# Kernel tuning notes

Measured on AMD Instinct MI355X. Metric: run time of the kernel, lower is better.

The kernel has to match this reference:

```python
import jax, jax.numpy as jnp
import numpy as np

B, S, D = 4, 4096, 1024
STATE = 1024
HID = 4 * D
EPS_NORM = 1e-6           # RMSNorm module eps
EPS_FP32 = 1.1920929e-7   # torch F.rms_norm default eps = finfo(fp32).eps


def rms_norm(x, eps):
    # no learned weight (RMSNorm(dim=-1) has weight=None)
    return x * jax.lax.rsqrt(jnp.mean(jnp.square(x), axis=-1, keepdims=True) + eps)


def setup_inputs() -> dict:
    key = jax.random.key(0)
    ks = jax.random.split(key, 8)
    scale_d = 1.0 / np.sqrt(D)
    scale_s = 1.0 / np.sqrt(STATE)
    scale_h = 1.0 / np.sqrt(HID)
    return {
        "x": jax.random.normal(ks[0], (B, S, D), jnp.float32),
        "x0": jax.random.normal(ks[1], (B, S, D), jnp.float32),
        "Wu": jax.random.normal(ks[2], (STATE, D), jnp.float32) * scale_d,
        "Wg": jax.random.normal(ks[3], (STATE, D), jnp.float32) * scale_d,
        "Wo": jax.random.normal(ks[4], (D, STATE), jnp.float32) * scale_s,
        "Wfc": jax.random.normal(ks[5], (HID, D), jnp.float32) * scale_d,
        "Wproj": jax.random.normal(ks[6], (D, HID), jnp.float32) * scale_h,
        "memory_mix": jnp.ones((D,), jnp.float32),
        "mlp_scale": jnp.ones((D,), jnp.float32),
        "resid_mix": jnp.stack([jnp.ones((D,), jnp.float32), jnp.zeros((D,), jnp.float32)]),
    }


def reference(x, x0, Wu, Wg, Wo, Wfc, Wproj, memory_mix, mlp_scale, resid_mix):
    # residual mix of x and x0
    x = resid_mix[0][None, None, :] * x + resid_mix[1][None, None, :] * x0

    # --- CausalPrefixMemory branch ---
    h = rms_norm(x, EPS_NORM)
    update = jnp.einsum('bsd,kd->bsk', h, Wu)
    gate = jax.nn.sigmoid(jnp.einsum('bsd,kd->bsk', h, Wg))
    memory = jnp.cumsum(gate * update, axis=1)          # [B,S,STATE]
    denom = jnp.arange(1, S + 1, dtype=jnp.float32)[None, :, None]
    m = rms_norm(memory / denom, EPS_FP32)
    mem_out = jnp.einsum('bsk,dk->bsd', m, Wo)
    x = x + memory_mix[None, None, :] * mem_out

    # --- MLP branch: relu^2 ---
    h2 = rms_norm(x, EPS_NORM)
    r = jax.nn.relu(jnp.einsum('bsd,hd->bsh', h2, Wfc))
    mlp_out = jnp.einsum('bsh,dh->bsd', jnp.square(r), Wproj)
    x = x + mlp_scale[None, None, :] * mlp_out
    return x
```

## Files before the change

kernel.cpp:

```cpp
#include <hip/hip_runtime.h>
#include <stdint.h>

typedef unsigned short u16;
typedef __attribute__((ext_vector_type(8))) short s16x8;
typedef __attribute__((ext_vector_type(4))) float f32x4;

__device__ __forceinline__ u16 f2bf(float f) {
  uint32_t u = __float_as_uint(f);
  uint32_t r = (u + 0x7FFFu + ((u >> 16) & 1u)) >> 16;
  return (u16)r;
}

__device__ __forceinline__ void gll16(const void* g, void* lds) {
  __builtin_amdgcn_global_load_lds(
      (const __attribute__((address_space(1))) uint32_t*)g,
      (__attribute__((address_space(3))) uint32_t*)lds, 16, 0, 0);
}

__device__ __forceinline__ void xcd_swz(int& bx, int& by) {
  int gx = gridDim.x;
  int lin = blockIdx.y * gx + blockIdx.x;
  int cpx = (gx * gridDim.y) >> 3;
  int nl = (lin & 7) * cpx + (lin >> 3);
  bx = nl % gx;
  by = nl / gx;
}

__global__ __launch_bounds__(256) void k_f2b(const float* __restrict__ src,
                                             u16* __restrict__ dst, int n) {
  int i = (blockIdx.x * 256 + threadIdx.x) * 4;
  if (i < n) {
    float4 v = *(const float4*)(src + i);
    ushort4 o;
    o.x = f2bf(v.x); o.y = f2bf(v.y); o.z = f2bf(v.z); o.w = f2bf(v.w);
    *(ushort4*)(dst + i) = o;
  }
}

template <bool MIX>
__global__ __launch_bounds__(256) void k_rms(const float* __restrict__ X,
                                             const float* __restrict__ X0,
                                             const float* __restrict__ rmix,
                                             float* __restrict__ XMout,
                                             u16* __restrict__ Hout, float eps) {
  const int row = blockIdx.x, t = threadIdx.x;
  const size_t base = (size_t)row * 1024;
  float4 v;
  if (MIX) {
    float4 a = ((const float4*)(X + base))[t];
    float4 b = ((const float4*)(X0 + base))[t];
    float4 c0 = ((const float4*)rmix)[t];
    float4 c1 = ((const float4*)(rmix + 1024))[t];
    v.x = c0.x * a.x + c1.x * b.x;
    v.y = c0.y * a.y + c1.y * b.y;
    v.z = c0.z * a.z + c1.z * b.z;
    v.w = c0.w * a.w + c1.w * b.w;
  } else {
    v = ((const float4*)(X + base))[t];
  }
  float ss = v.x * v.x + v.y * v.y + v.z * v.z + v.w * v.w;
#pragma unroll
  for (int o = 32; o > 0; o >>= 1) ss += __shfl_xor(ss, o);
  __shared__ float red[4];
  if ((t & 63) == 0) red[t >> 6] = ss;
  __syncthreads();
  float tot = red[0] + red[1] + red[2] + red[3];
  float sc = rsqrtf(tot * (1.0f / 1024.0f) + eps);
  if (MIX) ((float4*)(XMout + base))[t] = v;
  ushort4 hv;
  hv.x = f2bf(v.x * sc); hv.y = f2bf(v.y * sc);
  hv.z = f2bf(v.z * sc); hv.w = f2bf(v.w * sc);
  ((ushort4*)(Hout + base))[t] = hv;
}

__global__ __launch_bounds__(256) void k_scan2(float* __restrict__ CS) {
  int idx = blockIdx.x * 256 + threadIdx.x;
  int b = idx >> 10, k = idx & 1023;
  float run = 0.f;
  for (int c = 0; c < 256; ++c) {
    size_t o = ((size_t)b * 256 + c) * 1024 + k;
    float v = CS[o];
    CS[o] = run;
    run += v;
  }
}

__global__ __launch_bounds__(64) void k_scan3f(const float* __restrict__ P,
                                               const float* __restrict__ CS,
                                               u16* __restrict__ Mout) {
  int blk = blockIdx.x;
  int chunk = blk & 255, b = blk >> 8;
  const int t = threadIdx.x;
  const float4* cs4 = (const float4*)(CS + ((size_t)b * 256 + chunk) * 1024);
  float4 run[4];
#pragma unroll
  for (int q = 0; q < 4; ++q) run[q] = cs4[q * 64 + t];
  const float4* p4 = (const float4*)(P + ((size_t)b * 4096 + chunk * 16) * 1024);
  u16* mo = Mout + ((size_t)b * 4096 + chunk * 16) * 1024;
  const int rowbase = chunk * 16;
#pragma unroll 2
  for (int i = 0; i < 16; ++i) {
    float4 v[4];
#pragma unroll
    for (int q = 0; q < 4; ++q) v[q] = p4[(size_t)i * 256 + q * 64 + t];
    const float inv = 1.0f / (float)(rowbase + i + 1);
    float4 y[4];
    float ss = 0.f;
#pragma unroll
    for (int q = 0; q < 4; ++q) {
      run[q].x += v[q].x; run[q].y += v[q].y;
      run[q].z += v[q].z; run[q].w += v[q].w;
      y[q].x = run[q].x * inv; y[q].y = run[q].y * inv;
      y[q].z = run[q].z * inv; y[q].w = run[q].w * inv;
      ss += y[q].x * y[q].x + y[q].y * y[q].y
          + y[q].z * y[q].z + y[q].w * y[q].w;
    }
#pragma unroll
    for (int o = 32; o > 0; o >>= 1) ss += __shfl_xor(ss, o);
    float sc = rsqrtf(ss * (1.0f / 1024.0f) + 1.1920929e-7f);
#pragma unroll
    for (int q = 0; q < 4; ++q) {
      ushort4 hv;
      hv.x = f2bf(y[q].x * sc); hv.y = f2bf(y[q].y * sc);
      hv.z = f2bf(y[q].z * sc); hv.w = f2bf(y[q].w * sc);
      *(ushort4*)(mo + (size_t)i * 1024 + (q * 64 + t) * 4) = hv;
    }
  }
}

__global__ __launch_bounds__(256, 2) void gemm_dual(
    const u16* __restrict__ A, const u16* __restrict__ Bu,
    const u16* __restrict__ Bg, float* __restrict__ P,
    float* __restrict__ CS, int K) {
  __shared__ __align__(16) u16 As[128 * 64];
  __shared__ __align__(16) u16 Us[64 * 64];
  __shared__ __align__(16) u16 Gs[64 * 64];
  const int t = threadIdx.x;
  const int lane = t & 63, wid = t >> 6;
  int bx, by;
  xcd_swz(bx, by);
  const int m0 = by * 128, n0 = bx * 64;
  const int wm = wid * 32;
  const int l15 = lane & 15, lhi = lane >> 4;

  size_t gA[4], gU[2];
#pragma unroll
  for (int i = 0; i < 4; ++i) {
    int j = i * 256 + t;
    int row = j >> 3;
    int k16 = (j & 7) ^ (row & 7);
    gA[i] = (size_t)(m0 + row) * K + k16 * 8;
  }
#pragma unroll
  for (int i = 0; i < 2; ++i) {
    int j = i * 256 + t;
    int row = j >> 3;
    int k16 = (j & 7) ^ (row & 7);
    gU[i] = (size_t)(n0 + row) * K + k16 * 8;
  }

  f32x4 au[2][4], ag[2][4];
#pragma unroll
  for (int mi = 0; mi < 2; ++mi)
#pragma unroll
    for (int ni = 0; ni < 4; ++ni) { au[mi][ni] = 0.0f; ag[mi][ni] = 0.0f; }

  for (int kb = 0; kb < K; kb += 64) {
#pragma unroll
    for (int i = 0; i < 4; ++i) {
      int j = i * 256 + t;
      gll16(A + gA[i] + kb, &As[j * 8]);
    }
#pragma unroll
    for (int i = 0; i < 2; ++i) {
      int j = i * 256 + t;
      gll16(Bu + gU[i] + kb, &Us[j * 8]);
      gll16(Bg + gU[i] + kb, &Gs[j * 8]);
    }
    __syncthreads();
#pragma unroll
    for (int kc = 0; kc < 2; ++kc) {
      s16x8 af[2], uf[4], gf[4];
#pragma unroll
      for (int mi = 0; mi < 2; ++mi) {
        int row = wm + mi * 16 + l15;
        int k16 = (kc * 4 + lhi) ^ (row & 7);
        af[mi] = *(const s16x8*)&As[row * 64 + k16 * 8];
      }
#pragma unroll
      for (int ni = 0; ni < 4; ++ni) {
        int row = ni * 16 + l15;
        int k16 = (kc * 4 + lhi) ^ (row & 7);
        uf[ni] = *(const s16x8*)&Us[row * 64 + k16 * 8];
        gf[ni] = *(const s16x8*)&Gs[row * 64 + k16 * 8];
      }
#pragma unroll
      for (int mi = 0; mi < 2; ++mi)
#pragma unroll
        for (int ni = 0; ni < 4; ++ni) {
          au[mi][ni] = __builtin_amdgcn_mfma_f32_16x16x32_bf16(
              af[mi], uf[ni], au[mi][ni], 0, 0, 0);
          ag[mi][ni] = __builtin_amdgcn_mfma_f32_16x16x32_bf16(
              af[mi], gf[ni], ag[mi][ni], 0, 0, 0);
        }
    }
    __syncthreads();
  }

#pragma unroll
  for (int mi = 0; mi < 2; ++mi) {
    int r0 = m0 + wm + mi * 16 + lhi * 4;
#pragma unroll
    for (int ni = 0; ni < 4; ++ni) {
      int c = n0 + ni * 16 + l15;
      float ps = 0.f;
#pragma unroll
      for (int j = 0; j < 4; ++j) {
        float u = au[mi][ni][j], g = ag[mi][ni][j];
        float p = u / (1.0f + __expf(-g));
        P[(size_t)(r0 + j) * 1024 + c] = p;
        ps += p;
      }
      ps += __shfl_xor(ps, 16);
      ps += __shfl_xor(ps, 32);
      if (lhi == 0) {
        int grow = m0 + wm + mi * 16;
        int b = grow >> 12;
        int chunk = (grow & 4095) >> 4;
        CS[((size_t)b * 256 + chunk) * 1024 + c] = ps;
      }
    }
  }
}

template <int EPI>
__global__ __launch_bounds__(256, 2) void gemm_bf16(
    const u16* __restrict__ A, const u16* __restrict__ Bw, void* __restrict__ Cout,
    const float* __restrict__ Cadd, const float* __restrict__ colscale,
    int K, int lda, int ldb, int ldc) {
  __shared__ __align__(16) u16 As[128 * 64];
  __shared__ __align__(16) u16 Bs[128 * 64];
  const int t = threadIdx.x;
  const int lane = t & 63, wid = t >> 6;
  int bx, by;
  xcd_swz(bx, by);
  const int m0 = by * 128, n0 = bx * 128;
  const int wm = (wid >> 1) * 64, wn = (wid & 1) * 64;
  const int l15 = lane & 15, lhi = lane >> 4;

  size_t gA[4], gB[4];
#pragma unroll
  for (int i = 0; i < 4; ++i) {
    int j = i * 256 + t;
    int row = j >> 3;
    int k16 = (j & 7) ^ (row & 7);
    gA[i] = (size_t)(m0 + row) * lda + k16 * 8;
    gB[i] = (size_t)(n0 + row) * ldb + k16 * 8;
  }

  f32x4 acc[4][4];
#pragma unroll
  for (int mi = 0; mi < 4; ++mi)
#pragma unroll
    for (int ni = 0; ni < 4; ++ni) acc[mi][ni] = 0.0f;

  for (int kb = 0; kb < K; kb += 64) {
#pragma unroll
    for (int i = 0; i < 4; ++i) {
      int j = i * 256 + t;
      gll16(A + gA[i] + kb, &As[j * 8]);
      gll16(Bw + gB[i] + kb, &Bs[j * 8]);
    }
    __syncthreads();
#pragma unroll
    for (int kc = 0; kc < 2; ++kc) {
      s16x8 af[4], bfr[4];
#pragma unroll
      for (int mi = 0; mi < 4; ++mi) {
        int row = wm + mi * 16 + l15;
        int k16 = (kc * 4 + lhi) ^ (row & 7);
        af[mi] = *(const s16x8*)&As[row * 64 + k16 * 8];
      }
#pragma unroll
      for (int ni = 0; ni < 4; ++ni) {
        int row = wn + ni * 16 + l15;
        int k16 = (kc * 4 + lhi) ^ (row & 7);
        bfr[ni] = *(const s16x8*)&Bs[row * 64 + k16 * 8];
      }
#pragma unroll
      for (int mi = 0; mi < 4; ++mi)
#pragma unroll
        for (int ni = 0; ni < 4; ++ni)
          acc[mi][ni] = __builtin_amdgcn_mfma_f32_16x16x32_bf16(
              af[mi], bfr[ni], acc[mi][ni], 0, 0, 0);
    }
    __syncthreads();
  }

#pragma unroll
  for (int mi = 0; mi < 4; ++mi) {
    int r0 = m0 + wm + mi * 16 + lhi * 4;
#pragma unroll
    for (int ni = 0; ni < 4; ++ni) {
      int c = n0 + wn + ni * 16 + l15;
      float cs = (EPI == 1) ? colscale[c] : 0.f;
#pragma unroll
      for (int j = 0; j < 4; ++j) {
        size_t idx = (size_t)(r0 + j) * ldc + c;
        float v = acc[mi][ni][j];
        if (EPI == 1) {
          ((float*)Cout)[idx] = Cadd[idx] + cs * v;
        } else {
          float rv = fmaxf(v, 0.f);
          ((u16*)Cout)[idx] = f2bf(rv * rv);
        }
      }
    }
  }
}

extern "C" void kernel_launch(void* const* d_in, const int* in_sizes, int n_in,
                              void* d_out, int out_size, void* d_ws, size_t ws_size,
                              hipStream_t stream) {
  const float* x = (const float*)d_in[0];
  const float* x0 = (const float*)d_in[1];
  const float* Wu = (const float*)d_in[2];
  const float* Wg = (const float*)d_in[3];
  const float* Wo = (const float*)d_in[4];
  const float* Wfc = (const float*)d_in[5];
  const float* Wpj = (const float*)d_in[6];
  const float* mmix = (const float*)d_in[7];
  const float* mscale = (const float*)d_in[8];
  const float* rmix = (const float*)d_in[9];
  float* out = (float*)d_out;

  const int M = 16384;
  const size_t MiB = 1024 * 1024;

  char* ws = (char*)d_ws;
  u16* WuB = (u16*)ws;   ws += 2 * MiB;
  u16* WgB = (u16*)ws;   ws += 2 * MiB;
  u16* WoB = (u16*)ws;   ws += 2 * MiB;
  u16* WfcB = (u16*)ws;  ws += 8 * MiB;
  u16* WpjB = (u16*)ws;  ws += 8 * MiB;
  u16* h = (u16*)ws;     ws += 32 * MiB;
  char* pool = ws;
  float* P = (float*)pool;
  float* CS = (float*)(pool + 64 * MiB);
  u16* mB = (u16*)(pool + 68 * MiB);
  u16* R2 = (u16*)pool;
  float* xm = out;

  const bool fullR2 = ws_size >= 182 * MiB;

  k_f2b<<<1024, 256, 0, stream>>>(Wu, WuB, 1024 * 1024);
  k_f2b<<<1024, 256, 0, stream>>>(Wg, WgB, 1024 * 1024);
  k_f2b<<<1024, 256, 0, stream>>>(Wo, WoB, 1024 * 1024);
  k_f2b<<<4096, 256, 0, stream>>>(Wfc, WfcB, 4096 * 1024);
  k_f2b<<<4096, 256, 0, stream>>>(Wpj, WpjB, 4096 * 1024);

  k_rms<true><<<M, 256, 0, stream>>>(x, x0, rmix, xm, h, 1e-6f);

  gemm_dual<<<dim3(16, 128), 256, 0, stream>>>(h, WuB, WgB, P, CS, 1024);

  k_scan2<<<16, 256, 0, stream>>>(CS);
  k_scan3f<<<1024, 64, 0, stream>>>(P, CS, mB);

  gemm_bf16<1><<<dim3(8, 128), 256, 0, stream>>>(mB, WoB, xm, xm, mmix,
                                                 1024, 1024, 1024, 1024);
  k_rms<false><<<M, 256, 0, stream>>>(xm, nullptr, nullptr, nullptr, h, 1e-6f);

  if (fullR2) {
    gemm_bf16<2><<<dim3(32, 128), 256, 0, stream>>>(
        h, WfcB, R2, nullptr, nullptr, 1024, 1024, 1024, 4096);
    gemm_bf16<1><<<dim3(8, 128), 256, 0, stream>>>(
        R2, WpjB, out, out, mscale, 4096, 4096, 4096, 1024);
  } else {
    for (int c = 0; c < 2; ++c) {
      gemm_bf16<2><<<dim3(16, 128), 256, 0, stream>>>(
          h, WfcB + (size_t)c * 2048 * 1024, R2, nullptr, nullptr,
          1024, 1024, 1024, 2048);
      gemm_bf16<1><<<dim3(8, 128), 256, 0, stream>>>(
          R2, WpjB + (size_t)c * 2048, out, out, mscale,
          2048, 2048, 4096, 1024);
    }
  }
}
```

Measured before the change: 515.4 us.

## Store gated products in bf16, fuse weight conversions, vectorize scan kernels

The gated update intermediate P is now written as bf16 instead of fp32, which halves its write traffic in the dual GEMM and its read traffic in the scan kernel. The scan kernel reads 16-byte bf16 vectors and writes 16-byte outputs. The five weight-conversion launches are merged into one kernel that writes into the contiguous bf16 workspace. The chunk-prefix scan loads eight values at a time to expose memory-level parallelism. The cumulative sum now accumulates bf16-rounded values, which adds some precision risk.

Result: faster. 491.6 us (-4.6%).

```diff
diff --git a/kernel.cpp b/kernel.cpp
--- a/kernel.cpp
+++ b/kernel.cpp
@@ -9,6 +9,10 @@
   uint32_t u = __float_as_uint(f);
   uint32_t r = (u + 0x7FFFu + ((u >> 16) & 1u)) >> 16;
   return (u16)r;
+}
+
+__device__ __forceinline__ float bf2f(u16 h) {
+  return __uint_as_float((uint32_t)h << 16);
 }
 
 __device__ __forceinline__ void gll16(const void* g, void* lds) {
@@ -26,15 +30,22 @@
   by = nl / gx;
 }
 
-__global__ __launch_bounds__(256) void k_f2b(const float* __restrict__ src,
-                                             u16* __restrict__ dst, int n) {
-  int i = (blockIdx.x * 256 + threadIdx.x) * 4;
-  if (i < n) {
-    float4 v = *(const float4*)(src + i);
-    ushort4 o;
-    o.x = f2bf(v.x); o.y = f2bf(v.y); o.z = f2bf(v.z); o.w = f2bf(v.w);
-    *(ushort4*)(dst + i) = o;
-  }
+__global__ __launch_bounds__(256) void k_f2b5(
+    const float* __restrict__ s0, const float* __restrict__ s1,
+    const float* __restrict__ s2, const float* __restrict__ s3,
+    const float* __restrict__ s4, u16* __restrict__ dst) {
+  int i4 = blockIdx.x * 256 + threadIdx.x;
+  const float* src;
+  int base;
+  if (i4 < 262144)       { src = s0; base = 0; }
+  else if (i4 < 524288)  { src = s1; base = 262144; }
+  else if (i4 < 786432)  { src = s2; base = 524288; }
+  else if (i4 < 1835008) { src = s3; base = 786432; }
+  else                   { src = s4; base = 1835008; }
+  float4 v = ((const float4*)src)[i4 - base];
+  ushort4 o;
+  o.x = f2bf(v.x); o.y = f2bf(v.y); o.z = f2bf(v.z); o.w = f2bf(v.w);
+  ((ushort4*)dst)[i4] = o;
 }
 
 template <bool MIX>
@@ -77,15 +88,20 @@
   int idx = blockIdx.x * 256 + threadIdx.x;
   int b = idx >> 10, k = idx & 1023;
   float run = 0.f;
-  for (int c = 0; c < 256; ++c) {
-    size_t o = ((size_t)b * 256 + c) * 1024 + k;
-    float v = CS[o];
-    CS[o] = run;
-    run += v;
-  }
-}
-
-__global__ __launch_bounds__(64) void k_scan3f(const float* __restrict__ P,
+  for (int c0 = 0; c0 < 256; c0 += 8) {
+    float v[8];
+#pragma unroll
+    for (int j = 0; j < 8; ++j)
+      v[j] = CS[((size_t)b * 256 + c0 + j) * 1024 + k];
+#pragma unroll
+    for (int j = 0; j < 8; ++j) {
+      CS[((size_t)b * 256 + c0 + j) * 1024 + k] = run;
+      run += v[j];
+    }
+  }
+}
+
+__global__ __launch_bounds__(64) void k_scan3f(const u16* __restrict__ P,
                                                const float* __restrict__ CS,
                                                u16* __restrict__ Mout) {
   int blk = blockIdx.x;
@@ -93,44 +109,52 @@
   const int t = threadIdx.x;
   const float4* cs4 = (const float4*)(CS + ((size_t)b * 256 + chunk) * 1024);
   float4 run[4];
-#pragma unroll
-  for (int q = 0; q < 4; ++q) run[q] = cs4[q * 64 + t];
-  const float4* p4 = (const float4*)(P + ((size_t)b * 4096 + chunk * 16) * 1024);
+  run[0] = cs4[2 * t];       run[1] = cs4[2 * t + 1];
+  run[2] = cs4[128 + 2 * t]; run[3] = cs4[128 + 2 * t + 1];
+  const u16* pr = P + ((size_t)b * 4096 + chunk * 16) * 1024;
   u16* mo = Mout + ((size_t)b * 4096 + chunk * 16) * 1024;
   const int rowbase = chunk * 16;
 #pragma unroll 2
   for (int i = 0; i < 16; ++i) {
-    float4 v[4];
-#pragma unroll
-    for (int q = 0; q < 4; ++q) v[q] = p4[(size_t)i * 256 + q * 64 + t];
+    s16x8 c0 = *(const s16x8*)(pr + (size_t)i * 1024 + t * 8);
+    s16x8 c1 = *(const s16x8*)(pr + (size_t)i * 1024 + 512 + t * 8);
     const float inv = 1.0f / (float)(rowbase + i + 1);
-    float4 y[4];
+    float y[16];
     float ss = 0.f;
 #pragma unroll
-    for (int q = 0; q < 4; ++q) {
-      run[q].x += v[q].x; run[q].y += v[q].y;
-      run[q].z += v[q].z; run[q].w += v[q].w;
-      y[q].x = run[q].x * inv; y[q].y = run[q].y * inv;
-      y[q].z = run[q].z * inv; y[q].w = run[q].w * inv;
-      ss += y[q].x * y[q].x + y[q].y * y[q].y
-          + y[q].z * y[q].z + y[q].w * y[q].w;
-    }
+    for (int j = 0; j < 4; ++j) {
+      run[0][j] += bf2f((u16)c0[j]);
+      run[1][j] += bf2f((u16)c0[j + 4]);
+      run[2][j] += bf2f((u16)c1[j]);
+      run[3][j] += bf2f((u16)c1[j + 4]);
+    }
+#pragma unroll
+    for (int q = 0; q < 4; ++q)
+#pragma unroll
+      for (int j = 0; j < 4; ++j) {
+        float yy = run[q][j] * inv;
+        y[q * 4 + j] = yy;
+        ss += yy * yy;
+      }
 #pragma unroll
     for (int o = 32; o > 0; o >>= 1) ss += __shfl_xor(ss, o);
     float sc = rsqrtf(ss * (1.0f / 1024.0f) + 1.1920929e-7f);
-#pragma unroll
-    for (int q = 0; q < 4; ++q) {
-      ushort4 hv;
-      hv.x = f2bf(y[q].x * sc); hv.y = f2bf(y[q].y * sc);
-      hv.z = f2bf(y[q].z * sc); hv.w = f2bf(y[q].w * sc);
-      *(ushort4*)(mo + (size_t)i * 1024 + (q * 64 + t) * 4) = hv;
-    }
+    s16x8 o0, o1;
+#pragma unroll
+    for (int j = 0; j < 4; ++j) {
+      o0[j] = (short)f2bf(y[j] * sc);
+      o0[j + 4] = (short)f2bf(y[4 + j] * sc);
+      o1[j] = (short)f2bf(y[8 + j] * sc);
+      o1[j + 4] = (short)f2bf(y[12 + j] * sc);
+    }
+    *(s16x8*)(mo + (size_t)i * 1024 + t * 8) = o0;
+    *(s16x8*)(mo + (size_t)i * 1024 + 512 + t * 8) = o1;
   }
 }
 
 __global__ __launch_bounds__(256, 2) void gemm_dual(
     const u16* __restrict__ A, const u16* __restrict__ Bu,
-    const u16* __restrict__ Bg, float* __restrict__ P,
+    const u16* __restrict__ Bg, u16* __restrict__ P,
     float* __restrict__ CS, int K) {
   __shared__ __align__(16) u16 As[128 * 64];
   __shared__ __align__(16) u16 Us[64 * 64];
@@ -218,7 +242,7 @@
       for (int j = 0; j < 4; ++j) {
         float u = au[mi][ni][j], g = ag[mi][ni][j];
         float p = u / (1.0f + __expf(-g));
-        P[(size_t)(r0 + j) * 1024 + c] = p;
+        P[(size_t)(r0 + j) * 1024 + c] = f2bf(p);
         ps += p;
       }
       ps += __shfl_xor(ps, 16);
@@ -345,19 +369,15 @@
   u16* WpjB = (u16*)ws;  ws += 8 * MiB;
   u16* h = (u16*)ws;     ws += 32 * MiB;
   char* pool = ws;
-  float* P = (float*)pool;
-  float* CS = (float*)(pool + 64 * MiB);
-  u16* mB = (u16*)(pool + 68 * MiB);
+  u16* P = (u16*)pool;
+  float* CS = (float*)(pool + 32 * MiB);
+  u16* mB = (u16*)(pool + 36 * MiB);
   u16* R2 = (u16*)pool;
   float* xm = out;
 
   const bool fullR2 = ws_size >= 182 * MiB;
 
-  k_f2b<<<1024, 256, 0, stream>>>(Wu, WuB, 1024 * 1024);
-  k_f2b<<<1024, 256, 0, stream>>>(Wg, WgB, 1024 * 1024);
-  k_f2b<<<1024, 256, 0, stream>>>(Wo, WoB, 1024 * 1024);
-  k_f2b<<<4096, 256, 0, stream>>>(Wfc, WfcB, 4096 * 1024);
-  k_f2b<<<4096, 256, 0, stream>>>(Wpj, WpjB, 4096 * 1024);
+  k_f2b5<<<11264, 256, 0, stream>>>(Wu, Wg, Wo, Wfc, Wpj, WuB);
 
   k_rms<true><<<M, 256, 0, stream>>>(x, x0, rmix, xm, h, 1e-6f);
 
```
